# Performance work log

Measured on AMD Instinct MI355X. Metric: run time of the kernel, lower is better.

## Reference

```python
import jax, jax.numpy as jnp
import numpy as np


def setup_inputs() -> dict:
    key = jax.random.key(0)
    ks = jax.random.split(key, 11)
    C = 256
    s = 1.0 / np.sqrt(C)
    x = jax.random.normal(ks[0], (8, C, 128, 128), jnp.float32)
    v_w = jax.random.normal(ks[1], (C, C), jnp.float32) * s      # v_conv 1x1: C->C
    v_b = jax.random.normal(ks[2], (C,), jnp.float32) * 0.01
    k_w = jax.random.normal(ks[3], (C,), jnp.float32) * s        # k_conv 1x1: C->1
    k_b = jax.random.normal(ks[4], (), jnp.float32) * 0.01
    w1 = jax.random.normal(ks[5], (2,), jnp.float32) * 0.7       # conv1 1x1: 2->1 (h branch)
    b1 = jax.random.normal(ks[6], (), jnp.float32) * 0.01
    w2 = jax.random.normal(ks[7], (2,), jnp.float32) * 0.7       # conv2 1x1: 2->1 (w branch)
    b2 = jax.random.normal(ks[8], (), jnp.float32) * 0.01
    w3 = jax.random.normal(ks[9], (C,), jnp.float32) * s         # conv3 1x1: C->1
    b3 = jax.random.normal(ks[10], (), jnp.float32) * 0.01
    return dict(x=x, v_w=v_w, v_b=v_b, k_w=k_w, k_b=k_b,
                w1=w1, b1=b1, w2=w2, b2=b2, w3=w3, b3=b3)


def reference(x, v_w, v_b, k_w, k_b, w1, b1, w2, b2, w3, b3):
    b, c, h, w = x.shape
    # v_conv (1x1) and k_conv (1x1 -> single channel)
    tmp = jnp.einsum('oc,bchw->bohw', v_w, x) + v_b[None, :, None, None]
    k = (jnp.einsum('c,bchw->bhw', k_w, x) + k_b).reshape(b, h * w)
    k = jax.nn.softmax(k, axis=1)                                # softmax over spatial
    channel_fea = jnp.einsum('bcn,bn->bc', tmp.reshape(b, c, h * w), k)  # [b,c]
    # h branch: adaptive max/avg pool over (c, w) per height row
    h_max = jnp.max(x, axis=(1, 3))                              # [b,h]
    h_avg = jnp.mean(x, axis=(1, 3))                             # [b,h]
    h_att = jax.nn.sigmoid(w1[0] * h_max + w1[1] * h_avg + b1)   # [b,h]
    # w branch: adaptive max/avg pool over (c, h) per width column
    w_max = jnp.max(x, axis=(1, 2))                              # [b,w]
    w_avg = jnp.mean(x, axis=(1, 2))                             # [b,w]
    w_att = jax.nn.sigmoid(w2[0] * w_max + w2[1] * w_avg + b2)   # [b,w]
    # spatial_fea = h_att*tmp + w_att*tmp, fused as tmp*(h_att+w_att)
    spatial = tmp * (h_att[:, None, :, None] + w_att[:, None, None, :])
    s = jax.nn.sigmoid(jnp.einsum('c,bchw->bhw', w3, spatial) + b3)  # [b,h,w]
    return s[:, None, :, :] * channel_fea[:, :, None, None] + x
```

## Files before the change

### kernel.cpp

```cpp
#include <hip/hip_runtime.h>
#include <math.h>

#define CC 256
#define NN 16384
#define NB 8

#define WV3_OFF   0
#define WB3_OFF   256
#define S_OFF     257
#define KL_OFF    272
#define T3_OFF    (KL_OFF + NB*NN)
#define HSUM_OFF  (T3_OFF + NB*NN)
#define HMK_OFF   (HSUM_OFF + NB*128)
#define WSUM_OFF  (HMK_OFF + NB*128)
#define WMK_OFF   (WSUM_OFF + NB*128)
#define XK_OFF    (WMK_OFF + NB*128)
#define CF_OFF    (XK_OFF + NB*CC)
#define WS_FLOATS (CF_OFF + NB*CC)

__device__ __forceinline__ unsigned fkey(float f){
  unsigned b = __float_as_uint(f);
  return (b & 0x80000000u) ? ~b : (b ^ 0x80000000u);
}
__device__ __forceinline__ float fdekey(unsigned k){
  unsigned b = (k & 0x80000000u) ? (k ^ 0x80000000u) : ~k;
  return __uint_as_float(b);
}
__device__ __forceinline__ float sigmoidf_(float z){ return 1.0f/(1.0f+expf(-z)); }

__device__ __forceinline__ float blockReduceSum(float v, volatile float* lds){
  #pragma unroll
  for (int m=1;m<=32;m<<=1) v += __shfl_xor(v, m, 64);
  int wid = threadIdx.x>>6;
  __syncthreads();
  if ((threadIdx.x&63)==0) lds[wid] = v;
  __syncthreads();
  return lds[0]+lds[1]+lds[2]+lds[3];
}
__device__ __forceinline__ float blockReduceMax(float v, volatile float* lds){
  #pragma unroll
  for (int m=1;m<=32;m<<=1) v = fmaxf(v, __shfl_xor(v, m, 64));
  int wid = threadIdx.x>>6;
  __syncthreads();
  if ((threadIdx.x&63)==0) lds[wid] = v;
  __syncthreads();
  return fmaxf(fmaxf(lds[0],lds[1]), fmaxf(lds[2],lds[3]));
}

__global__ __launch_bounds__(256) void k0(const float* __restrict__ v_w,
                                          const float* __restrict__ v_b,
                                          const float* __restrict__ w3,
                                          float* __restrict__ ws){
  int t = threadIdx.x;
  float acc = 0.f;
  for (int o=0;o<CC;++o) acc += w3[o]*v_w[o*CC + t];
  ws[WV3_OFF + t] = acc;
  __shared__ float lds[4];
  float tot = blockReduceSum(w3[t]*v_b[t], lds);
  if (t==0) ws[WB3_OFF] = tot;
}

__global__ __launch_bounds__(256) void k1(const float* __restrict__ x,
                                          const float* __restrict__ k_w,
                                          float* __restrict__ ws)
{
  const int t    = threadIdx.x;
  const int tile = blockIdx.x;
  const int cc   = blockIdx.y;
  const int b    = blockIdx.z;
  const int n0   = tile*1024;
  const int c0   = cc*64;

  __shared__ float skw[64], swv[64];
  __shared__ float lws[4][128], lwm[4][128];
  __shared__ float lhs[8], lhm[8];
  if (t < 64){ skw[t] = k_w[c0+t]; swv[t] = ws[WV3_OFF + c0 + t]; }
  __syncthreads();

  float kla[4]={0,0,0,0}, t3a[4]={0,0,0,0}, cs[4]={0,0,0,0};
  float cm[4]={-INFINITY,-INFINITY,-INFINITY,-INFINITY};

  const float* xb = x + ((size_t)(b*CC + c0))*NN + n0 + t*4;
  #pragma unroll 4
  for (int c=0;c<64;++c){
    const float4 v = *(const float4*)(xb + (size_t)c*NN);
    const float kw = skw[c], wv = swv[c];
    kla[0] += kw*v.x; kla[1] += kw*v.y; kla[2] += kw*v.z; kla[3] += kw*v.w;
    t3a[0] += wv*v.x; t3a[1] += wv*v.y; t3a[2] += wv*v.z; t3a[3] += wv*v.w;
    cs[0] += v.x; cs[1] += v.y; cs[2] += v.z; cs[3] += v.w;
    cm[0] = fmaxf(cm[0], v.x); cm[1] = fmaxf(cm[1], v.y);
    cm[2] = fmaxf(cm[2], v.z); cm[3] = fmaxf(cm[3], v.w);
  }

  {
    float* klp = ws + KL_OFF + (size_t)b*NN + n0 + t*4;
    float* t3p = ws + T3_OFF + (size_t)b*NN + n0 + t*4;
    atomicAdd(klp+0, kla[0]); atomicAdd(klp+1, kla[1]);
    atomicAdd(klp+2, kla[2]); atomicAdd(klp+3, kla[3]);
    atomicAdd(t3p+0, t3a[0]); atomicAdd(t3p+1, t3a[1]);
    atomicAdd(t3p+2, t3a[2]); atomicAdd(t3p+3, t3a[3]);
  }

  float hs = cs[0]+cs[1]+cs[2]+cs[3];
  float hm = fmaxf(fmaxf(cm[0],cm[1]), fmaxf(cm[2],cm[3]));
  #pragma unroll
  for (int m=1;m<=16;m<<=1){
    hs += __shfl_xor(hs, m, 64);
    hm  = fmaxf(hm, __shfl_xor(hm, m, 64));
  }
  const int lane = t & 63, wid = t >> 6;
  if ((lane & 31) == 0){ lhs[t>>5] = hs; lhm[t>>5] = hm; }

  #pragma unroll
  for (int j=0;j<4;++j){
    cs[j] += __shfl_xor(cs[j], 32, 64);
    cm[j]  = fmaxf(cm[j], __shfl_xor(cm[j], 32, 64));
  }
  if (lane < 32){
    #pragma unroll
    for (int j=0;j<4;++j){ lws[wid][lane*4+j] = cs[j]; lwm[wid][lane*4+j] = cm[j]; }
  }
  __syncthreads();

  if (t < 128){
    float s = lws[0][t]+lws[1][t]+lws[2][t]+lws[3][t];
    float m = fmaxf(fmaxf(lwm[0][t],lwm[1][t]), fmaxf(lwm[2][t],lwm[3][t]));
    atomicAdd(ws + WSUM_OFF + b*128 + t, s);
    atomicMax((unsigned*)ws + WMK_OFF + b*128 + t, fkey(m));
  } else if (t < 136){
    int r = t - 128;
    atomicAdd(ws + HSUM_OFF + b*128 + tile*8 + r, lhs[r]);
    atomicMax((unsigned*)ws + HMK_OFF + b*128 + tile*8 + r, fkey(lhm[r]));
  }
}

__global__ __launch_bounds__(256) void k2(float* __restrict__ ws,
                                          const float* __restrict__ w1, const float* __restrict__ b1,
                                          const float* __restrict__ w2, const float* __restrict__ b2,
                                          const float* __restrict__ b3)
{
  const int b = blockIdx.x, t = threadIdx.x;
  __shared__ float lds[4];
  __shared__ float ha[128], wa[128];
  float* kl = ws + KL_OFF + (size_t)b*NN;

  float m = -INFINITY;
  for (int j=t; j<NN; j+=256) m = fmaxf(m, kl[j]);
  m = blockReduceMax(m, lds);

  float s = 0.f;
  for (int j=t; j<NN; j+=256){ float e = expf(kl[j]-m); kl[j] = e; s += e; }
  s = blockReduceSum(s, lds);
  if (t==0) ws[S_OFF + b] = s;

  if (t < 128){
    float hsum = ws[HSUM_OFF + b*128 + t] * (1.0f/(256.0f*128.0f));
    float hmax = fdekey(((unsigned*)ws)[HMK_OFF + b*128 + t]);
    ha[t] = sigmoidf_(w1[0]*hmax + w1[1]*hsum + b1[0]);
  } else {
    int w = t - 128;
    float wsum = ws[WSUM_OFF + b*128 + w] * (1.0f/(256.0f*128.0f));
    float wmax = fdekey(((unsigned*)ws)[WMK_OFF + b*128 + w]);
    wa[w] = sigmoidf_(w2[0]*wmax + w2[1]*wsum + b2[0]);
  }
  __syncthreads();

  const float wb3 = ws[WB3_OFF], bb3 = b3[0];
  float* t3 = ws + T3_OFF + (size_t)b*NN;
  for (int j=t; j<NN; j+=256){
    float att = ha[j>>7] + wa[j&127];
    float tv  = t3[j] + wb3;
    t3[j] = sigmoidf_(att*tv + bb3);
  }
}

__global__ __launch_bounds__(256) void k3(const float* __restrict__ x,
                                          float* __restrict__ ws){
  const int c = blockIdx.x, b = blockIdx.y, t = threadIdx.x;
  const float4* x4 = (const float4*)(x + ((size_t)(b*CC + c))*NN);
  const float4* e4 = (const float4*)(ws + KL_OFF + (size_t)b*NN);
  float acc = 0.f;
  #pragma unroll 4
  for (int j=t; j<NN/4; j+=256){
    float4 xv = x4[j], ev = e4[j];
    acc += xv.x*ev.x + xv.y*ev.y + xv.z*ev.z + xv.w*ev.w;
  }
  __shared__ float lds[4];
  acc = blockReduceSum(acc, lds);
  if (t==0) ws[XK_OFF + b*CC + c] = acc;
}

__global__ __launch_bounds__(256) void k4(const float* __restrict__ v_w,
                                          const float* __restrict__ v_b,
                                          float* __restrict__ ws){
  const int b = blockIdx.x, t = threadIdx.x;
  __shared__ float xks[CC];
  const float Sinv = 1.0f / ws[S_OFF + b];
  xks[t] = ws[XK_OFF + b*CC + t] * Sinv;
  __syncthreads();
  float acc = v_b[t];
  for (int c=0;c<CC;++c) acc += v_w[t*CC + c]*xks[c];
  ws[CF_OFF + b*CC + t] = acc;
}

__global__ __launch_bounds__(256) void k5(const float* __restrict__ x,
                                          const float* __restrict__ ws,
                                          float* __restrict__ out){
  const float4* x4 = (const float4*)x;
  float4* o4 = (float4*)out;
  const float4* s4 = (const float4*)(ws + T3_OFF);
  const float* cf = ws + CF_OFF;
  const int nq = NB*CC*NN/4;
  for (int q = blockIdx.x*256 + threadIdx.x; q < nq; q += gridDim.x*256){
    int bc = q >> 12;
    int b  = bc >> 8;
    int n4 = q & 4095;
    float f = cf[bc];
    float4 sv = s4[(size_t)b*4096 + n4];
    float4 xv = x4[q];
    float4 r;
    r.x = sv.x*f + xv.x; r.y = sv.y*f + xv.y;
    r.z = sv.z*f + xv.z; r.w = sv.w*f + xv.w;
    o4[q] = r;
  }
}

extern "C" void kernel_launch(void* const* d_in, const int* in_sizes, int n_in,
                              void* d_out, int out_size, void* d_ws, size_t ws_size,
                              hipStream_t stream) {
  const float* x   = (const float*)d_in[0];
  const float* v_w = (const float*)d_in[1];
  const float* v_b = (const float*)d_in[2];
  const float* k_w = (const float*)d_in[3];
  const float* w1  = (const float*)d_in[5];
  const float* b1  = (const float*)d_in[6];
  const float* w2  = (const float*)d_in[7];
  const float* b2  = (const float*)d_in[8];
  const float* w3  = (const float*)d_in[9];
  const float* b3  = (const float*)d_in[10];
  float* ws  = (float*)d_ws;
  float* out = (float*)d_out;

  hipMemsetAsync(d_ws, 0, (size_t)WS_FLOATS*sizeof(float), stream);
  k0<<<1, 256, 0, stream>>>(v_w, v_b, w3, ws);
  k1<<<dim3(16,4,NB), 256, 0, stream>>>(x, k_w, ws);
  k2<<<NB, 256, 0, stream>>>(ws, w1, b1, w2, b2, b3);
  k3<<<dim3(CC,NB), 256, 0, stream>>>(x, ws);
  k4<<<NB, 256, 0, stream>>>(v_w, v_b, ws);
  k5<<<2048, 256, 0, stream>>>(x, ws, out);
}
```

Baseline: 363.1 us.

## Fuse softmax-weighted channel reduction into first pass and sigmoid into output kernel

The spatial softmax is computed without max subtraction, and the x·exp(k) channel reduction moves into k1. That kernel now re-reads its own x tile, with one block per (batch, 512-column tile) spanning all channels, so k2 and k3 and their full extra pass over x go away. The spatial sigmoid gating is deferred into the final elementwise kernel using per-row and per-column attention vectors. k0 is split over 16 blocks with atomics. The unnormalised exp risks overflow for large logits, and the coarser k1 grid with per-channel wave shuffles may lower occupancy.

```diff
diff --git a/kernel.cpp b/kernel.cpp
--- a/kernel.cpp
+++ b/kernel.cpp
@@ -1,22 +1,25 @@
 #include <hip/hip_runtime.h>
 #include <math.h>
 
-#define CC 256
-#define NN 16384
-#define NB 8
+#define CC   256
+#define NN   16384
+#define NB   8
+#define TILE 512
+#define NT   32
 
 #define WV3_OFF   0
 #define WB3_OFF   256
-#define S_OFF     257
-#define KL_OFF    272
-#define T3_OFF    (KL_OFF + NB*NN)
-#define HSUM_OFF  (T3_OFF + NB*NN)
-#define HMK_OFF   (HSUM_OFF + NB*128)
-#define WSUM_OFF  (HMK_OFF + NB*128)
-#define WMK_OFF   (WSUM_OFF + NB*128)
-#define XK_OFF    (WMK_OFF + NB*128)
-#define CF_OFF    (XK_OFF + NB*CC)
-#define WS_FLOATS (CF_OFF + NB*CC)
+#define S_OFF     264
+#define HSUM_OFF  272
+#define HMAX_OFF  1296
+#define WSUM_OFF  2320
+#define WMK_OFF   3344
+#define XK_OFF    4368
+#define CF_OFF    6416
+#define HA_OFF    8464
+#define WA_OFF    9488
+#define T3_OFF    10512
+#define ZERO_BYTES (6416*4)
 
 __device__ __forceinline__ unsigned fkey(float f){
   unsigned b = __float_as_uint(f);
@@ -27,200 +30,170 @@
   return __uint_as_float(b);
 }
 __device__ __forceinline__ float sigmoidf_(float z){ return 1.0f/(1.0f+expf(-z)); }
-
-__device__ __forceinline__ float blockReduceSum(float v, volatile float* lds){
-  #pragma unroll
-  for (int m=1;m<=32;m<<=1) v += __shfl_xor(v, m, 64);
-  int wid = threadIdx.x>>6;
-  __syncthreads();
-  if ((threadIdx.x&63)==0) lds[wid] = v;
-  __syncthreads();
-  return lds[0]+lds[1]+lds[2]+lds[3];
-}
-__device__ __forceinline__ float blockReduceMax(float v, volatile float* lds){
-  #pragma unroll
-  for (int m=1;m<=32;m<<=1) v = fmaxf(v, __shfl_xor(v, m, 64));
-  int wid = threadIdx.x>>6;
-  __syncthreads();
-  if ((threadIdx.x&63)==0) lds[wid] = v;
-  __syncthreads();
-  return fmaxf(fmaxf(lds[0],lds[1]), fmaxf(lds[2],lds[3]));
-}
 
 __global__ __launch_bounds__(256) void k0(const float* __restrict__ v_w,
                                           const float* __restrict__ v_b,
                                           const float* __restrict__ w3,
                                           float* __restrict__ ws){
-  int t = threadIdx.x;
+  const int t = threadIdx.x, g = blockIdx.x;
   float acc = 0.f;
-  for (int o=0;o<CC;++o) acc += w3[o]*v_w[o*CC + t];
-  ws[WV3_OFF + t] = acc;
-  __shared__ float lds[4];
-  float tot = blockReduceSum(w3[t]*v_b[t], lds);
-  if (t==0) ws[WB3_OFF] = tot;
+  #pragma unroll
+  for (int i=0;i<16;++i){
+    int o = g*16 + i;
+    acc += w3[o]*v_w[o*CC + t];
+  }
+  atomicAdd(ws + WV3_OFF + t, acc);
+  if (g == 0){
+    float v = w3[t]*v_b[t];
+    #pragma unroll
+    for (int m=1;m<=32;m<<=1) v += __shfl_xor(v, m, 64);
+    __shared__ float l[4];
+    if ((t&63)==0) l[t>>6] = v;
+    __syncthreads();
+    if (t==0) ws[WB3_OFF] = l[0]+l[1]+l[2]+l[3];
+  }
 }
 
 __global__ __launch_bounds__(256) void k1(const float* __restrict__ x,
                                           const float* __restrict__ k_w,
                                           float* __restrict__ ws)
 {
-  const int t    = threadIdx.x;
-  const int tile = blockIdx.x;
-  const int cc   = blockIdx.y;
-  const int b    = blockIdx.z;
-  const int n0   = tile*1024;
-  const int c0   = cc*64;
-
-  __shared__ float skw[64], swv[64];
-  __shared__ float lws[4][128], lwm[4][128];
-  __shared__ float lhs[8], lhm[8];
-  if (t < 64){ skw[t] = k_w[c0+t]; swv[t] = ws[WV3_OFF + c0 + t]; }
-  __syncthreads();
-
-  float kla[4]={0,0,0,0}, t3a[4]={0,0,0,0}, cs[4]={0,0,0,0};
-  float cm[4]={-INFINITY,-INFINITY,-INFINITY,-INFINITY};
-
-  const float* xb = x + ((size_t)(b*CC + c0))*NN + n0 + t*4;
-  #pragma unroll 4
-  for (int c=0;c<64;++c){
-    const float4 v = *(const float4*)(xb + (size_t)c*NN);
-    const float kw = skw[c], wv = swv[c];
-    kla[0] += kw*v.x; kla[1] += kw*v.y; kla[2] += kw*v.z; kla[3] += kw*v.w;
-    t3a[0] += wv*v.x; t3a[1] += wv*v.y; t3a[2] += wv*v.z; t3a[3] += wv*v.w;
-    cs[0] += v.x; cs[1] += v.y; cs[2] += v.z; cs[3] += v.w;
-    cm[0] = fmaxf(cm[0], v.x); cm[1] = fmaxf(cm[1], v.y);
-    cm[2] = fmaxf(cm[2], v.z); cm[3] = fmaxf(cm[3], v.w);
-  }
-
-  {
-    float* klp = ws + KL_OFF + (size_t)b*NN + n0 + t*4;
-    float* t3p = ws + T3_OFF + (size_t)b*NN + n0 + t*4;
-    atomicAdd(klp+0, kla[0]); atomicAdd(klp+1, kla[1]);
-    atomicAdd(klp+2, kla[2]); atomicAdd(klp+3, kla[3]);
-    atomicAdd(t3p+0, t3a[0]); atomicAdd(t3p+1, t3a[1]);
-    atomicAdd(t3p+2, t3a[2]); atomicAdd(t3p+3, t3a[3]);
-  }
-
-  float hs = cs[0]+cs[1]+cs[2]+cs[3];
-  float hm = fmaxf(fmaxf(cm[0],cm[1]), fmaxf(cm[2],cm[3]));
-  #pragma unroll
-  for (int m=1;m<=16;m<<=1){
+  const int t = threadIdx.x, lane = t&63, wv = t>>6;
+  const int tile = blockIdx.x, b = blockIdx.y;
+  const int n0 = tile*TILE;
+
+  __shared__ float skw[CC], swv[CC];
+  __shared__ float lred[4][128];
+  __shared__ float sS[4];
+  skw[t] = k_w[t];
+  swv[t] = ws[WV3_OFF + t];
+  __syncthreads();
+
+  const float* xb = x + (size_t)b*CC*NN + n0 + 2*t;
+
+  float kl0=0.f,kl1=0.f,t30=0.f,t31=0.f,cs0=0.f,cs1=0.f;
+  float cm0=-INFINITY, cm1=-INFINITY;
+  #pragma unroll 8
+  for (int c=0;c<CC;++c){
+    const float2 v = *(const float2*)(xb + (size_t)c*NN);
+    const float kw = skw[c], wvv = swv[c];
+    kl0 += kw*v.x;  kl1 += kw*v.y;
+    t30 += wvv*v.x; t31 += wvv*v.y;
+    cs0 += v.x;     cs1 += v.y;
+    cm0 = fmaxf(cm0, v.x); cm1 = fmaxf(cm1, v.y);
+  }
+
+  *(float2*)(ws + T3_OFF + (size_t)b*NN + n0 + 2*t) = make_float2(t30, t31);
+
+  float hs = cs0+cs1, hm = fmaxf(cm0, cm1);
+  #pragma unroll
+  for (int m=1;m<=32;m<<=1){
     hs += __shfl_xor(hs, m, 64);
     hm  = fmaxf(hm, __shfl_xor(hm, m, 64));
   }
-  const int lane = t & 63, wid = t >> 6;
-  if ((lane & 31) == 0){ lhs[t>>5] = hs; lhm[t>>5] = hm; }
-
-  #pragma unroll
-  for (int j=0;j<4;++j){
-    cs[j] += __shfl_xor(cs[j], 32, 64);
-    cm[j]  = fmaxf(cm[j], __shfl_xor(cm[j], 32, 64));
-  }
-  if (lane < 32){
-    #pragma unroll
-    for (int j=0;j<4;++j){ lws[wid][lane*4+j] = cs[j]; lwm[wid][lane*4+j] = cm[j]; }
-  }
-  __syncthreads();
-
+  if (lane == 0){
+    ws[HSUM_OFF + b*128 + tile*4 + wv] = hs;
+    ws[HMAX_OFF + b*128 + tile*4 + wv] = hm;
+  }
+
+  lred[wv][2*lane] = cs0; lred[wv][2*lane+1] = cs1;
+  __syncthreads();
+  if (t < 128)
+    atomicAdd(ws + WSUM_OFF + b*128 + t, lred[0][t]+lred[1][t]+lred[2][t]+lred[3][t]);
+  __syncthreads();
+  lred[wv][2*lane] = cm0; lred[wv][2*lane+1] = cm1;
+  __syncthreads();
   if (t < 128){
-    float s = lws[0][t]+lws[1][t]+lws[2][t]+lws[3][t];
-    float m = fmaxf(fmaxf(lwm[0][t],lwm[1][t]), fmaxf(lwm[2][t],lwm[3][t]));
-    atomicAdd(ws + WSUM_OFF + b*128 + t, s);
-    atomicMax((unsigned*)ws + WMK_OFF + b*128 + t, fkey(m));
-  } else if (t < 136){
-    int r = t - 128;
-    atomicAdd(ws + HSUM_OFF + b*128 + tile*8 + r, lhs[r]);
-    atomicMax((unsigned*)ws + HMK_OFF + b*128 + tile*8 + r, fkey(lhm[r]));
-  }
-}
-
-__global__ __launch_bounds__(256) void k2(float* __restrict__ ws,
+    float m_ = fmaxf(fmaxf(lred[0][t],lred[1][t]), fmaxf(lred[2][t],lred[3][t]));
+    atomicMax((unsigned*)ws + WMK_OFF + b*128 + t, fkey(m_));
+  }
+
+  const float e0 = expf(kl0), e1 = expf(kl1);
+  float es = e0 + e1;
+  #pragma unroll
+  for (int m=1;m<=32;m<<=1) es += __shfl_xor(es, m, 64);
+  if (lane == 0) sS[wv] = es;
+  __syncthreads();
+  if (t == 0) atomicAdd(ws + S_OFF + b, sS[0]+sS[1]+sS[2]+sS[3]);
+
+  float xkacc0=0.f, xkacc1=0.f, xkacc2=0.f, xkacc3=0.f;
+  #pragma unroll
+  for (int cg=0; cg<4; ++cg){
+    #pragma unroll 8
+    for (int cl=0; cl<64; ++cl){
+      const int c = cg*64 + cl;
+      const float2 v = *(const float2*)(xb + (size_t)c*NN);
+      float p = v.x*e0 + v.y*e1;
+      #pragma unroll
+      for (int m=1;m<=32;m<<=1) p += __shfl_xor(p, m, 64);
+      if (lane == cl){
+        if      (cg==0) xkacc0 = p;
+        else if (cg==1) xkacc1 = p;
+        else if (cg==2) xkacc2 = p;
+        else            xkacc3 = p;
+      }
+    }
+  }
+  atomicAdd(ws + XK_OFF + b*CC +   0 + lane, xkacc0);
+  atomicAdd(ws + XK_OFF + b*CC +  64 + lane, xkacc1);
+  atomicAdd(ws + XK_OFF + b*CC + 128 + lane, xkacc2);
+  atomicAdd(ws + XK_OFF + b*CC + 192 + lane, xkacc3);
+}
+
+__global__ __launch_bounds__(256) void k4(const float* __restrict__ v_w,
+                                          const float* __restrict__ v_b,
                                           const float* __restrict__ w1, const float* __restrict__ b1,
                                           const float* __restrict__ w2, const float* __restrict__ b2,
-                                          const float* __restrict__ b3)
-{
+                                          float* __restrict__ ws){
   const int b = blockIdx.x, t = threadIdx.x;
-  __shared__ float lds[4];
-  __shared__ float ha[128], wa[128];
-  float* kl = ws + KL_OFF + (size_t)b*NN;
-
-  float m = -INFINITY;
-  for (int j=t; j<NN; j+=256) m = fmaxf(m, kl[j]);
-  m = blockReduceMax(m, lds);
-
-  float s = 0.f;
-  for (int j=t; j<NN; j+=256){ float e = expf(kl[j]-m); kl[j] = e; s += e; }
-  s = blockReduceSum(s, lds);
-  if (t==0) ws[S_OFF + b] = s;
-
+  const float inv = 1.0f/(256.0f*128.0f);
   if (t < 128){
-    float hsum = ws[HSUM_OFF + b*128 + t] * (1.0f/(256.0f*128.0f));
-    float hmax = fdekey(((unsigned*)ws)[HMK_OFF + b*128 + t]);
-    ha[t] = sigmoidf_(w1[0]*hmax + w1[1]*hsum + b1[0]);
+    float hsum = ws[HSUM_OFF + b*128 + t] * inv;
+    float hmax = ws[HMAX_OFF + b*128 + t];
+    ws[HA_OFF + b*128 + t] = sigmoidf_(w1[0]*hmax + w1[1]*hsum + b1[0]);
   } else {
     int w = t - 128;
-    float wsum = ws[WSUM_OFF + b*128 + w] * (1.0f/(256.0f*128.0f));
+    float wsum = ws[WSUM_OFF + b*128 + w] * inv;
     float wmax = fdekey(((unsigned*)ws)[WMK_OFF + b*128 + w]);
-    wa[w] = sigmoidf_(w2[0]*wmax + w2[1]*wsum + b2[0]);
-  }
-  __syncthreads();
-
-  const float wb3 = ws[WB3_OFF], bb3 = b3[0];
-  float* t3 = ws + T3_OFF + (size_t)b*NN;
-  for (int j=t; j<NN; j+=256){
-    float att = ha[j>>7] + wa[j&127];
-    float tv  = t3[j] + wb3;
-    t3[j] = sigmoidf_(att*tv + bb3);
-  }
-}
-
-__global__ __launch_bounds__(256) void k3(const float* __restrict__ x,
-                                          float* __restrict__ ws){
-  const int c = blockIdx.x, b = blockIdx.y, t = threadIdx.x;
-  const float4* x4 = (const float4*)(x + ((size_t)(b*CC + c))*NN);
-  const float4* e4 = (const float4*)(ws + KL_OFF + (size_t)b*NN);
-  float acc = 0.f;
-  #pragma unroll 4
-  for (int j=t; j<NN/4; j+=256){
-    float4 xv = x4[j], ev = e4[j];
-    acc += xv.x*ev.x + xv.y*ev.y + xv.z*ev.z + xv.w*ev.w;
-  }
-  __shared__ float lds[4];
-  acc = blockReduceSum(acc, lds);
-  if (t==0) ws[XK_OFF + b*CC + c] = acc;
-}
-
-__global__ __launch_bounds__(256) void k4(const float* __restrict__ v_w,
-                                          const float* __restrict__ v_b,
-                                          float* __restrict__ ws){
-  const int b = blockIdx.x, t = threadIdx.x;
+    ws[WA_OFF + b*128 + w] = sigmoidf_(w2[0]*wmax + w2[1]*wsum + b2[0]);
+  }
   __shared__ float xks[CC];
   const float Sinv = 1.0f / ws[S_OFF + b];
   xks[t] = ws[XK_OFF + b*CC + t] * Sinv;
   __syncthreads();
   float acc = v_b[t];
+  #pragma unroll 8
   for (int c=0;c<CC;++c) acc += v_w[t*CC + c]*xks[c];
   ws[CF_OFF + b*CC + t] = acc;
 }
 
 __global__ __launch_bounds__(256) void k5(const float* __restrict__ x,
                                           const float* __restrict__ ws,
+                                          const float* __restrict__ b3,
                                           float* __restrict__ out){
   const float4* x4 = (const float4*)x;
   float4* o4 = (float4*)out;
-  const float4* s4 = (const float4*)(ws + T3_OFF);
+  const float4* t34 = (const float4*)(ws + T3_OFF);
+  const float4* wa4 = (const float4*)(ws + WA_OFF);
+  const float* ha = ws + HA_OFF;
   const float* cf = ws + CF_OFF;
+  const float wb3 = ws[WB3_OFF];
+  const float bb3 = b3[0];
   const int nq = NB*CC*NN/4;
   for (int q = blockIdx.x*256 + threadIdx.x; q < nq; q += gridDim.x*256){
-    int bc = q >> 12;
-    int b  = bc >> 8;
-    int n4 = q & 4095;
-    float f = cf[bc];
-    float4 sv = s4[(size_t)b*4096 + n4];
-    float4 xv = x4[q];
+    const int bc = q >> 12;
+    const int b  = bc >> 8;
+    const int n4 = q & 4095;
+    const float f = cf[bc];
+    const float hav = ha[b*128 + (n4>>5)];
+    const float4 wav = wa4[b*32 + (n4&31)];
+    const float4 tv = t34[(size_t)b*4096 + n4];
+    const float4 xv = x4[q];
     float4 r;
-    r.x = sv.x*f + xv.x; r.y = sv.y*f + xv.y;
-    r.z = sv.z*f + xv.z; r.w = sv.w*f + xv.w;
+    r.x = sigmoidf_((hav+wav.x)*(tv.x+wb3)+bb3)*f + xv.x;
+    r.y = sigmoidf_((hav+wav.y)*(tv.y+wb3)+bb3)*f + xv.y;
+    r.z = sigmoidf_((hav+wav.z)*(tv.z+wb3)+bb3)*f + xv.z;
+    r.w = sigmoidf_((hav+wav.w)*(tv.w+wb3)+bb3)*f + xv.w;
     o4[q] = r;
   }
 }
@@ -241,11 +214,9 @@
   float* ws  = (float*)d_ws;
   float* out = (float*)d_out;
 
-  hipMemsetAsync(d_ws, 0, (size_t)WS_FLOATS*sizeof(float), stream);
-  k0<<<1, 256, 0, stream>>>(v_w, v_b, w3, ws);
-  k1<<<dim3(16,4,NB), 256, 0, stream>>>(x, k_w, ws);
-  k2<<<NB, 256, 0, stream>>>(ws, w1, b1, w2, b2, b3);
-  k3<<<dim3(CC,NB), 256, 0, stream>>>(x, ws);
-  k4<<<NB, 256, 0, stream>>>(v_w, v_b, ws);
-  k5<<<2048, 256, 0, stream>>>(x, ws, out);
-}
+  hipMemsetAsync(d_ws, 0, ZERO_BYTES, stream);
+  k0<<<16, 256, 0, stream>>>(v_w, v_b, w3, ws);
+  k1<<<dim3(NT, NB), 256, 0, stream>>>(x, k_w, ws);
+  k4<<<NB, 256, 0, stream>>>(v_w, v_b, w1, b1, w2, b2, ws);
+  k5<<<2048, 256, 0, stream>>>(x, ws, b3, out);
+}
```

After: 325.2 us. 10.4% less time.
